# Performance work log

Measured on AMD Instinct MI355X. Metric: run time of the kernel, lower is better.

The kernel has to match this reference:

```python
import jax, jax.numpy as jnp
import numpy as np

SEQ = 2048
DIM = 4096
N_HEADS = 32
N_KV_HEADS = 8
HEAD_DIM = DIM // N_HEADS  # 128
ROPE_THETA = 500000.0


def setup_inputs() -> dict:
    key = jax.random.key(0)
    ks = jax.random.split(key, 5)
    s = 0.02  # keep activations numerically tame
    return {
        "x": jax.random.normal(ks[0], (SEQ, DIM), dtype=jnp.float32),
        "wq": jax.random.normal(ks[1], (DIM, DIM), dtype=jnp.float32) * s,
        "wk": jax.random.normal(ks[2], (N_KV_HEADS * HEAD_DIM, DIM), dtype=jnp.float32) * s,
        "wv": jax.random.normal(ks[3], (N_KV_HEADS * HEAD_DIM, DIM), dtype=jnp.float32) * s,
        "wo": jax.random.normal(ks[4], (DIM, DIM), dtype=jnp.float32) * s,
    }


def _rope(t):
    # t: [S, H, D]; pairs (t[...,2i], t[...,2i+1]) rotated by angle pos * theta^(-i/(D/2)),
    # matching torch.view_as_complex on x.view(S, -1, 2) * polar(1, pos*freq).
    S, H, D = t.shape
    half = D // 2
    freqs = 1.0 / (ROPE_THETA ** (jnp.arange(half, dtype=jnp.float32) / half))
    ang = jnp.arange(S, dtype=jnp.float32)[:, None] * freqs[None, :]  # [S, half]
    cos = jnp.cos(ang)[:, None, :]  # [S, 1, half]
    sin = jnp.sin(ang)[:, None, :]
    tr = t.reshape(S, H, half, 2)
    x0, x1 = tr[..., 0], tr[..., 1]
    r0 = x0 * cos - x1 * sin
    r1 = x0 * sin + x1 * cos
    return jnp.stack([r0, r1], axis=-1).reshape(S, H, D)


def reference(x, wq, wk, wv, wo):
    S = x.shape[0]
    group = N_HEADS // N_KV_HEADS
    # Per-head projections (batched over heads instead of python loop)
    q = jnp.einsum("sd,hkd->shk", x, wq.reshape(N_HEADS, HEAD_DIM, DIM))        # [S,H,D]
    k = jnp.einsum("sd,hkd->shk", x, wk.reshape(N_KV_HEADS, HEAD_DIM, DIM))     # [S,Hkv,D]
    v = jnp.einsum("sd,hkd->shk", x, wv.reshape(N_KV_HEADS, HEAD_DIM, DIM))     # [S,Hkv,D]
    q = _rope(q)
    k = _rope(k)
    # GQA: q head h uses kv head h // group -> repeat kv heads consecutively
    kf = jnp.repeat(k, group, axis=1)  # [S,H,D]
    vf = jnp.repeat(v, group, axis=1)  # [S,H,D]
    scores = jnp.einsum("shd,thd->hst", q, kf) / jnp.sqrt(jnp.float32(HEAD_DIM))
    causal = jnp.tril(jnp.ones((S, S), dtype=bool))
    scores = jnp.where(causal[None], scores, -jnp.inf)
    probs = jax.nn.softmax(scores, axis=-1)
    out = jnp.einsum("hst,thd->shd", probs, vf).reshape(S, N_HEADS * HEAD_DIM)
    return out @ wo.T
```

## Files before the change

### kernel.cpp

```cpp
#include <hip/hip_runtime.h>
#include <stdint.h>
#include <math.h>

#define SEQ   2048
#define DIM   4096
#define NHEAD 32
#define NKV   8
#define HD    128
#define KVDIM (NKV*HD)

typedef __bf16 bf16x8 __attribute__((ext_vector_type(8)));
typedef float  f32x4  __attribute__((ext_vector_type(4)));

__device__ __forceinline__ uint16_t f2bf(float f) {
  uint32_t u = __float_as_uint(f);
  uint32_t r = (u + 0x7FFFu + ((u >> 16) & 1u)) >> 16;
  return (uint16_t)r;
}
__device__ __forceinline__ bf16x8 ld_frag(const uint16_t* p) {
  return *(const bf16x8*)p;
}
__device__ __forceinline__ void async_cp16(const void* g, void* lds) {
  __builtin_amdgcn_global_load_lds(
      (const __attribute__((address_space(1))) void*)g,
      (__attribute__((address_space(3))) void*)lds, 16, 0, 0);
}
__device__ __forceinline__ uint32_t lds_u32(const void* p) {
  return (uint32_t)(uintptr_t)(const __attribute__((address_space(3))) void*)p;
}
__device__ __forceinline__ bf16x8 ds_read_b128a(uint32_t addr) {
  f32x4 r;
  asm volatile("ds_read_b128 %0, %1" : "=v"(r) : "v"(addr));
  return __builtin_bit_cast(bf16x8, r);
}

__global__ __launch_bounds__(256) void k_conv_all(
    const float* __restrict__ x, const float* __restrict__ wq,
    const float* __restrict__ wk, const float* __restrict__ wv,
    uint16_t* __restrict__ xb, uint16_t* __restrict__ wqkvb) {
  size_t i = (size_t)blockIdx.x * 256 + threadIdx.x;
  const float* s; uint16_t* d; size_t off;
  if (i < 2097152)      { s = x;  d = xb;                 off = i; }
  else if (i < 6291456) { s = wq; d = wqkvb;              off = i - 2097152; }
  else if (i < 7340032) { s = wk; d = wqkvb + 16777216u;  off = i - 6291456; }
  else                  { s = wv; d = wqkvb + 20971520u;  off = i - 7340032; }
  const float4 v = ((const float4*)s)[off];
  ushort4 o;
  o.x = f2bf(v.x); o.y = f2bf(v.y); o.z = f2bf(v.z); o.w = f2bf(v.w);
  ((ushort4*)d)[off] = o;
}

__global__ __launch_bounds__(256) void k_conv(const float* __restrict__ s,
                                              uint16_t* __restrict__ d, int n4) {
  int i = blockIdx.x * 256 + threadIdx.x;
  if (i >= n4) return;
  const float4 v = ((const float4*)s)[i];
  ushort4 o;
  o.x = f2bf(v.x); o.y = f2bf(v.y); o.z = f2bf(v.z); o.w = f2bf(v.w);
  ((ushort4*)d)[i] = o;
}


#define STG32(Tn) do {                                                          \
    const int _rg = ((Tn) & 3) * 8192;                                          \
    async_cp16(gA + (size_t)crow * DIM + (size_t)(Tn) * 32 + cs * 8,            \
               sA + _rg + tid * 8);                                             \
    async_cp16(gA + (size_t)(crow + 128) * DIM + (size_t)(Tn) * 32 + cs * 8,    \
               sA + _rg + 4096 + tid * 8);                                      \
    async_cp16(gB + (size_t)crow * DIM + (size_t)(Tn) * 32 + cs * 8,            \
               sB + _rg + tid * 8);                                             \
    async_cp16(gB + (size_t)(crow + 128) * DIM + (size_t)(Tn) * 32 + cs * 8,    \
               sB + _rg + 4096 + tid * 8);                                      \
  } while (0)

#define READ12(AF, BF, ringoff) do {                                            \
    _Pragma("unroll")                                                           \
    for (int _t = 0; _t < 8; _t++) AF[_t] = ds_read_b128a(offA[_t] + (ringoff));\
    _Pragma("unroll")                                                           \
    for (int _u = 0; _u < 4; _u++) BF[_u] = ds_read_b128a(offB[_u] + (ringoff));\
  } while (0)

#define MFMA32(AF, BF)                                                          \
    _Pragma("unroll")                                                           \
    for (int _t = 0; _t < 8; _t++)                                              \
      _Pragma("unroll")                                                         \
      for (int _u = 0; _u < 4; _u++)                                            \
        acc[_t][_u] = __builtin_amdgcn_mfma_f32_16x16x32_bf16(AF[_t], BF[_u],   \
                                                              acc[_t][_u], 0, 0, 0);

#define BODY(CA, CB, NA, NB, T) do {                                            \
    if ((T) + 3 < 128) STG32((T) + 3);                                          \
    if ((T) + 1 < 128) {                                                        \
      const uint32_t _ro = (uint32_t)((((T) + 1) & 3) << 14);                   \
      READ12(NA, NB, _ro);                                                      \
      asm volatile("s_waitcnt lgkmcnt(12)" ::: "memory");                       \
    } else {                                                                    \
      asm volatile("s_waitcnt lgkmcnt(0)" ::: "memory");                        \
    }                                                                           \
    __builtin_amdgcn_sched_barrier(0);                                          \
    __builtin_amdgcn_s_setprio(1);                                              \
    MFMA32(CA, CB);                                                             \
    __builtin_amdgcn_s_setprio(0);                                              \
    if ((T) + 3 < 128) { asm volatile("s_waitcnt vmcnt(4)" ::: "memory"); }     \
    else               { asm volatile("s_waitcnt vmcnt(0)" ::: "memory"); }     \
    if ((T) < 127) __builtin_amdgcn_s_barrier();                                \
  } while (0)

#define G256_PROLOGUE(Aptr, Bptr)                                               \
  __shared__ __align__(16) uint16_t sA[4 * 8192];                               \
  __shared__ __align__(16) uint16_t sB[4 * 8192];                               \
  const int tid  = threadIdx.x;                                                 \
  const int lane = tid & 63;                                                    \
  const int wv   = tid >> 6;                                                    \
  const int quad = lane >> 4;                                                   \
  const int l16  = lane & 15;                                                   \
  const int wm   = (wv >> 2) << 7;                                \
  const int wn   = (wv & 3) << 6;                             \
  const uint16_t* gA = Aptr + (size_t)m0 * DIM;                                 \
  const uint16_t* gB = Bptr + (size_t)n0 * DIM;                                 \
  const int crow = tid >> 2;                                                    \
  const int cs   = (tid & 3) ^ ((crow >> 1) & 3);                               \
  const uint32_t sAb = lds_u32(sA);                                             \
  const uint32_t sBb = lds_u32(sB);                                             \
  uint32_t offA[8], offB[4];                                                    \
  _Pragma("unroll")                                                             \
  for (int t = 0; t < 8; t++) {                                                 \
    int r_ = wm + t * 16 + l16;                                                 \
    offA[t] = sAb + (uint32_t)(r_ * 64 + (quad ^ ((r_ >> 1) & 3)) * 16);        \
  }                                                                             \
  _Pragma("unroll")                                                             \
  for (int u = 0; u < 4; u++) {                                                 \
    int r_ = wn + u * 16 + l16;                                                 \
    offB[u] = sBb + (uint32_t)(r_ * 64 + (quad ^ ((r_ >> 1) & 3)) * 16);        \
  }                                                                             \
  f32x4 acc[8][4] = {};                                                         \
  bf16x8 afC[8], bfC[4], afN[8], bfN[4];                                        \
  STG32(0); STG32(1); STG32(2);                                                 \
  asm volatile("s_waitcnt vmcnt(4)" ::: "memory");        \
  __builtin_amdgcn_s_barrier();                                                 \
  READ12(afC, bfC, 0u);                                                         \
  for (int T = 0; T < 128; T += 2) {                                            \
    BODY(afC, bfC, afN, bfN, T);                                                \
    BODY(afN, bfN, afC, bfC, T + 1);                                            \
  }

__global__ __launch_bounds__(512, 2) void k_gemm_qkv(
    const uint16_t* __restrict__ xb, const uint16_t* __restrict__ wqkvb,
    uint16_t* __restrict__ Qb, uint16_t* __restrict__ Kb, uint16_t* __restrict__ Vb)
{
  const int bx = blockIdx.x;
  const int m0 = blockIdx.y * 256;
  const int n0 = bx * 256;
  G256_PROLOGUE(xb, wqkvb)

  const int region = (bx < 16) ? 0 : (bx < 20 ? 1 : 2);
  uint16_t* outp; int ldC, cbase;
  if (region == 0)      { outp = Qb; ldC = DIM;   cbase = n0; }
  else if (region == 1) { outp = Kb; ldC = KVDIM; cbase = n0 - 4096; }
  else                  { outp = Vb; ldC = KVDIM; cbase = n0 - 5120; }

  #pragma unroll
  for (int t = 0; t < 8; t++)
    #pragma unroll
    for (int u = 0; u < 4; u++) {
      const int col = cbase + wn + u * 16 + l16;
      const int d = col & 127;
      const float freq = expf(-0.20503693f * (float)(d >> 1));
      const float sgn = (d & 1) ? 1.0f : -1.0f;
      #pragma unroll
      for (int r = 0; r < 4; r++) {
        const int row = m0 + wm + t * 16 + quad * 4 + r;
        float v = acc[t][u][r];
        if (region < 2) {
          float p = __shfl_xor(v, 1, 64);
          float ang = (float)row * freq;
          float sn, cc2;
          sincosf(ang, &sn, &cc2);
          v = v * cc2 + p * sn * sgn;
        }
        outp[(size_t)row * ldC + col] = f2bf(v);
      }
    }
}

__global__ __launch_bounds__(512, 2) void k_gemm_o(
    const uint16_t* __restrict__ ab, const uint16_t* __restrict__ wob,
    float* __restrict__ out)
{
  const int m0 = blockIdx.y * 256;
  const int n0 = blockIdx.x * 256;
  G256_PROLOGUE(ab, wob)
  #pragma unroll
  for (int t = 0; t < 8; t++)
    #pragma unroll
    for (int u = 0; u < 4; u++)
      #pragma unroll
      for (int r = 0; r < 4; r++) {
        int row = m0 + wm + t * 16 + quad * 4 + r;
        int col = n0 + wn + u * 16 + l16;
        out[(size_t)row * DIM + col] = acc[t][u][r];
      }
}

__global__ __launch_bounds__(256) void k_vtrans(const uint16_t* __restrict__ Vb,
                                                uint16_t* __restrict__ VT) {
  __shared__ uint16_t t[64][72];
  const int s0 = blockIdx.x * 64;
  const int c0 = blockIdx.y * 64;
  const int tid = threadIdx.x;
  #pragma unroll
  for (int i = 0; i < 2; i++) {
    int idx = i * 256 + tid;
    int r = idx >> 3, ch = idx & 7;
    uint4 dv = *(const uint4*)(Vb + (size_t)(s0 + r) * KVDIM + c0 + ch * 8);
    *(uint4*)(&t[r][ch * 8]) = dv;
  }
  __syncthreads();
  const int kvh = c0 >> 7;
  const int dbase = c0 & 127;
  #pragma unroll
  for (int i = 0; i < 2; i++) {
    int idx = i * 256 + tid;
    int d = idx >> 3, sc = idx & 7;
    uint16_t tmp[8];
    #pragma unroll
    for (int j2 = 0; j2 < 8; j2++) tmp[j2] = t[sc * 8 + j2][d];
    *(uint4*)(VT + (size_t)kvh * HD * SEQ + (size_t)(dbase + d) * SEQ + s0 + sc * 8) = *(const uint4*)tmp;
  }
}

#define BKV 64
#define NPAIR 40
__device__ __constant__ uint8_t c_pair[NPAIR] = {
  12,16,20,24,28,29,32,33,36,37,40,41,44,45,46,48,49,50,52,53,54,56,57,58,60,61,62,63,
  8,25,42,59,
  4,21,38,55,
  0,17,34,51
};
__device__ __constant__ uint8_t c_base[16] = {0,1,2,3,4,6,8,10,12,15,18,21,24,28,32,36};

__global__ __launch_bounds__(256) void k_flash_split(
    const uint16_t* __restrict__ Qb, const uint16_t* __restrict__ Kb,
    const uint16_t* __restrict__ VT, uint16_t* __restrict__ Opart,
    float* __restrict__ ml)
{
  const int pair = c_pair[blockIdx.x];
  const int qt   = pair >> 2;
  const int seg  = pair & 3;
  const int h    = blockIdx.y;
  const int kvh  = h >> 2;
  const int slot = h * NPAIR + c_base[qt] + seg;
  const int tid  = threadIdx.x;
  const int lane = tid & 63;
  const int wv   = tid >> 6;
  const int quad = lane >> 4;
  const int l16  = lane & 15;
  const int q0   = qt * 128;

  __shared__ __align__(16) uint16_t sK[BKV * 128];
  __shared__ __align__(16) uint16_t sVT[HD * BKV];
  __shared__ __align__(16) uint16_t sP[4 * 32 * 72];

  const uint16_t* Kbase  = Kb + kvh * HD;
  const uint16_t* VTbase = VT + (size_t)kvh * HD * SEQ;

  bf16x8 qf[2][4];
  #pragma unroll
  for (int mt = 0; mt < 2; mt++)
    #pragma unroll
    for (int ks = 0; ks < 4; ks++)
      qf[mt][ks] = ld_frag(Qb + (size_t)(q0 + wv * 32 + mt * 16 + l16) * DIM + h * HD + ks * 32 + quad * 8);

  __align__(16) uint16_t ones_bits[8];
  #pragma unroll
  for (int j = 0; j < 8; j++) ones_bits[j] = (l16 == 0) ? 0x3F80 : 0;
  const bf16x8 onesf = *(const bf16x8*)ones_bits;

  f32x4 Oacc[2][8] = {};
  f32x4 Lacc[2] = {};

  const float scale = 0.08838834764831845f;
  const float MFIX = 12.0f;
  const int j0 = seg * 8;
  const int j1 = min(j0 + 8, 2 * (qt + 1));

  for (int j = j0; j < j1; j++) {
    const int t0 = j * BKV;
    #pragma unroll
    for (int i = 0; i < 4; i++) {
      int pos = i * 256 + tid;
      int row = pos >> 4, g = (pos & 15) ^ (row & 7);
      async_cp16(Kbase + (size_t)(t0 + row) * KVDIM + g * 8, sK + pos * 8);
      int vrow = pos >> 3, vg = (pos & 7) ^ (vrow & 7);
      async_cp16(VTbase + (size_t)vrow * SEQ + t0 + vg * 8, sVT + pos * 8);
    }
    __syncthreads();

    bool active = (t0 <= q0 + wv * 32 + 31);
    if (active) {
      f32x4 Sacc[2][4] = {};
      #pragma unroll
      for (int ks = 0; ks < 4; ks++) {
        bf16x8 kf[4];
        #pragma unroll
        for (int nt = 0; nt < 4; nt++)
          kf[nt] = ld_frag(sK + (nt * 16 + l16) * 128 + (((ks * 4 + quad) ^ (l16 & 7)) * 8));
        #pragma unroll
        for (int mt = 0; mt < 2; mt++)
          #pragma unroll
          for (int nt = 0; nt < 4; nt++)
            Sacc[mt][nt] = __builtin_amdgcn_mfma_f32_16x16x32_bf16(qf[mt][ks], kf[nt], Sacc[mt][nt], 0, 0, 0);
      }
      const bool diag = (t0 + BKV - 1) > (q0 + wv * 32);
      #pragma unroll
      for (int mt = 0; mt < 2; mt++)
        #pragma unroll
        for (int nt = 0; nt < 4; nt++)
          #pragma unroll
          for (int r = 0; r < 4; r++) {
            float sv = Sacc[mt][nt][r] * scale - MFIX;
            bool msk = false;
            if (diag) {
              int qg = q0 + wv * 32 + mt * 16 + quad * 4 + r;
              int tg = t0 + nt * 16 + l16;
              msk = tg > qg;
            }
            float pv = msk ? 0.0f : __expf(sv);
            sP[(wv * 32 + mt * 16 + quad * 4 + r) * 72 + nt * 16 + l16] = f2bf(pv);
          }
      #pragma unroll
      for (int ks = 0; ks < 2; ks++) {
        bf16x8 pf[2], vf[8];
        #pragma unroll
        for (int mt = 0; mt < 2; mt++)
          pf[mt] = ld_frag(sP + (wv * 32 + mt * 16 + l16) * 72 + ks * 32 + quad * 8);
        #pragma unroll
        for (int dt = 0; dt < 8; dt++)
          vf[dt] = ld_frag(sVT + (dt * 16 + l16) * 64 + (((ks * 4 + quad) ^ (l16 & 7)) * 8));
        #pragma unroll
        for (int mt = 0; mt < 2; mt++) {
          Lacc[mt] = __builtin_amdgcn_mfma_f32_16x16x32_bf16(pf[mt], onesf, Lacc[mt], 0, 0, 0);
          #pragma unroll
          for (int dt = 0; dt < 8; dt++)
            Oacc[mt][dt] = __builtin_amdgcn_mfma_f32_16x16x32_bf16(pf[mt], vf[dt], Oacc[mt][dt], 0, 0, 0);
        }
      }
    }
    __syncthreads();
  }

  uint16_t* Op = Opart + (size_t)slot * (128 * 128);
  #pragma unroll
  for (int mt = 0; mt < 2; mt++)
    #pragma unroll
    for (int r = 0; r < 4; r++) {
      int row = wv * 32 + mt * 16 + quad * 4 + r;
      #pragma unroll
      for (int dt = 0; dt < 8; dt++)
        Op[row * 128 + dt * 16 + l16] = f2bf(Oacc[mt][dt][r]);
      if (l16 == 0)
        ml[(size_t)slot * 128 + row] = Lacc[mt][r];
    }
}

__global__ __launch_bounds__(256) void k_combine(
    const uint16_t* __restrict__ Opart, const float* __restrict__ ml,
    uint16_t* __restrict__ attnb)
{
  const int qt = blockIdx.x;
  const int h  = blockIdx.y;
  const int nseg = (qt >> 2) + 1;
  const int slot0 = h * NPAIR + c_base[qt];
  const int tid = threadIdx.x;
  const int row = tid >> 1;
  const int dh  = (tid & 1) * 64;

  float L = 0.0f;
  #pragma unroll
  for (int i = 0; i < 4; i++)
    if (i < nseg) L += ml[(size_t)(slot0 + i) * 128 + row];
  const float invL = 1.0f / L;

  uint16_t* dst = attnb + (size_t)(qt * 128 + row) * DIM + h * HD + dh;
  #pragma unroll
  for (int c = 0; c < 8; c++) {
    int d = dh + c * 8;
    float acc[8] = {};
    #pragma unroll
    for (int i = 0; i < 4; i++) {
      if (i < nseg) {
        bf16x8 v = ld_frag(Opart + (size_t)(slot0 + i) * (128 * 128) + row * 128 + d);
        #pragma unroll
        for (int j = 0; j < 8; j++) acc[j] += (float)v[j];
      }
    }
    uint16_t outv[8];
    #pragma unroll
    for (int j = 0; j < 8; j++) outv[j] = f2bf(acc[j] * invL);
    *(uint4*)(dst + c * 8) = *(const uint4*)outv;
  }
}

extern "C" void kernel_launch(void* const* d_in, const int* in_sizes, int n_in,
                              void* d_out, int out_size, void* d_ws, size_t ws_size,
                              hipStream_t stream) {
  const float* x  = (const float*)d_in[0];
  const float* wq = (const float*)d_in[1];
  const float* wk = (const float*)d_in[2];
  const float* wv = (const float*)d_in[3];
  const float* wo = (const float*)d_in[4];
  float* out = (float*)d_out;

  uint8_t* ws = (uint8_t*)d_ws;
  uint16_t* xb     = (uint16_t*)(ws + 0);
  uint16_t* wqkvb  = (uint16_t*)(ws + 16777216ull);
  uint16_t* Qb     = (uint16_t*)(ws + 67108864ull);
  uint16_t* Kb     = (uint16_t*)(ws + 83886080ull);
  uint16_t* Vb     = (uint16_t*)(ws + 88080384ull);
  uint16_t* VT     = (uint16_t*)(ws + 16777216ull);
  uint16_t* Opart  = (uint16_t*)(ws + 20971520ull);
  float*    mlbuf  = (float*)   (ws + 62914560ull);
  uint16_t* wob    = (uint16_t*)(ws + 16777216ull);
  uint16_t* attnb  = xb;

  k_conv_all<<<32768, 256, 0, stream>>>(x, wq, wk, wv, xb, wqkvb);
  k_gemm_qkv<<<dim3(24, 8), 512, 0, stream>>>(xb, wqkvb, Qb, Kb, Vb);
  k_vtrans<<<dim3(32, 16), 256, 0, stream>>>(Vb, VT);
  k_flash_split<<<dim3(NPAIR, 32), 256, 0, stream>>>(Qb, Kb, VT, Opart, mlbuf);
  k_combine<<<dim3(16, 32), 256, 0, stream>>>(Opart, mlbuf, attnb);
  k_conv<<<16384, 256, 0, stream>>>(wo, wob, 4194304);
  k_gemm_o<<<dim3(16, 8), 512, 0, stream>>>(attnb, wob, out);
}
```

Before: 611.5 us.

## Rewrite output-projection GEMM with 128x256 tiles and 4-stage async LDS pipeline

The O-projection GEMM moves from 256x256 tiles on 128 blocks to 128x256 tiles on 256 blocks, so more of the GPU's compute units get work. It adds a custom 4-buffer async global-to-LDS pipeline that keeps three stages in flight. Fragment reads are double-buffered in registers and timed with explicit waitcnt and sched barriers, and MFMA issue priority is raised. Smaller tiles re-read more of the A and B operands, and the hand-scheduled wait counts add a correctness risk if they are wrong.

```diff
diff --git a/kernel.cpp b/kernel.cpp
--- a/kernel.cpp
+++ b/kernel.cpp
@@ -183,15 +183,93 @@
     }
 }
 
+
+#define O_STG(Tn) do {                                                          \
+    const int _ra = ((Tn) & 3) * 4096;                                          \
+    const int _rb = ((Tn) & 3) * 8192;                                          \
+    async_cp16(gA + (size_t)crow * DIM + (size_t)(Tn) * 32 + cs * 8,            \
+               sA + _ra + tid * 8);                                             \
+    async_cp16(gB + (size_t)crow * DIM + (size_t)(Tn) * 32 + cs * 8,            \
+               sB + _rb + tid * 8);                                             \
+    async_cp16(gB + (size_t)(crow + 128) * DIM + (size_t)(Tn) * 32 + cs * 8,    \
+               sB + _rb + 4096 + tid * 8);                                      \
+  } while (0)
+
+#define O_BODY(CA, CB, NA, NB, T) do {                                          \
+    if ((T) + 3 < 128) O_STG((T) + 3);                                          \
+    if ((T) + 1 < 128) {                                                        \
+      const uint32_t _ra = (uint32_t)((((T) + 1) & 3) << 13);                   \
+      const uint32_t _rb = (uint32_t)((((T) + 1) & 3) << 14);                   \
+      _Pragma("unroll")                                                         \
+      for (int _t = 0; _t < 4; _t++) NA[_t] = ds_read_b128a(offA[_t] + _ra);    \
+      _Pragma("unroll")                                                         \
+      for (int _u = 0; _u < 4; _u++) NB[_u] = ds_read_b128a(offB[_u] + _rb);    \
+      asm volatile("s_waitcnt lgkmcnt(8)" ::: "memory");                        \
+    } else {                                                                    \
+      asm volatile("s_waitcnt lgkmcnt(0)" ::: "memory");                        \
+    }                                                                           \
+    __builtin_amdgcn_sched_barrier(0);                                          \
+    __builtin_amdgcn_s_setprio(1);                                              \
+    _Pragma("unroll")                                                           \
+    for (int _t = 0; _t < 4; _t++)                                              \
+      _Pragma("unroll")                                                         \
+      for (int _u = 0; _u < 4; _u++)                                            \
+        acc[_t][_u] = __builtin_amdgcn_mfma_f32_16x16x32_bf16(CA[_t], CB[_u],   \
+                                                              acc[_t][_u], 0, 0, 0); \
+    __builtin_amdgcn_s_setprio(0);                                              \
+    if ((T) + 3 < 128) { asm volatile("s_waitcnt vmcnt(3)" ::: "memory"); }     \
+    else               { asm volatile("s_waitcnt vmcnt(0)" ::: "memory"); }     \
+    if ((T) < 127) __builtin_amdgcn_s_barrier();                                \
+  } while (0)
+
 __global__ __launch_bounds__(512, 2) void k_gemm_o(
     const uint16_t* __restrict__ ab, const uint16_t* __restrict__ wob,
     float* __restrict__ out)
 {
-  const int m0 = blockIdx.y * 256;
+  __shared__ __align__(16) uint16_t sA[4 * 4096];
+  __shared__ __align__(16) uint16_t sB[4 * 8192];
+  const int m0 = blockIdx.y * 128;
   const int n0 = blockIdx.x * 256;
-  G256_PROLOGUE(ab, wob)
-  #pragma unroll
-  for (int t = 0; t < 8; t++)
+  const int tid  = threadIdx.x;
+  const int lane = tid & 63;
+  const int wv   = tid >> 6;
+  const int quad = lane >> 4;
+  const int l16  = lane & 15;
+  const int wm   = (wv >> 2) << 6;
+  const int wn   = (wv & 3) << 6;
+  const uint16_t* gA = ab  + (size_t)m0 * DIM;
+  const uint16_t* gB = wob + (size_t)n0 * DIM;
+  const int crow = tid >> 2;
+  const int cs   = (tid & 3) ^ ((crow >> 1) & 3);
+  const uint32_t sAb = lds_u32(sA);
+  const uint32_t sBb = lds_u32(sB);
+  uint32_t offA[4], offB[4];
+  #pragma unroll
+  for (int t = 0; t < 4; t++) {
+    int r_ = wm + t * 16 + l16;
+    offA[t] = sAb + (uint32_t)(r_ * 64 + (quad ^ ((r_ >> 1) & 3)) * 16);
+  }
+  #pragma unroll
+  for (int u = 0; u < 4; u++) {
+    int r_ = wn + u * 16 + l16;
+    offB[u] = sBb + (uint32_t)(r_ * 64 + (quad ^ ((r_ >> 1) & 3)) * 16);
+  }
+  f32x4 acc[4][4] = {};
+  bf16x8 afC[4], bfC[4], afN[4], bfN[4];
+  O_STG(0); O_STG(1); O_STG(2);
+  asm volatile("s_waitcnt vmcnt(3)" ::: "memory");
+  __builtin_amdgcn_s_barrier();
+  #pragma unroll
+  for (int _t = 0; _t < 4; _t++) afC[_t] = ds_read_b128a(offA[_t]);
+  #pragma unroll
+  for (int _u = 0; _u < 4; _u++) bfC[_u] = ds_read_b128a(offB[_u]);
+  for (int T = 0; T < 128; T += 2) {
+    O_BODY(afC, bfC, afN, bfN, T);
+    O_BODY(afN, bfN, afC, bfC, T + 1);
+  }
+  asm volatile("s_waitcnt vmcnt(0)" ::: "memory");
+  #pragma unroll
+  for (int t = 0; t < 4; t++)
     #pragma unroll
     for (int u = 0; u < 4; u++)
       #pragma unroll
@@ -429,5 +507,5 @@
   k_flash_split<<<dim3(NPAIR, 32), 256, 0, stream>>>(Qb, Kb, VT, Opart, mlbuf);
   k_combine<<<dim3(16, 32), 256, 0, stream>>>(Opart, mlbuf, attnb);
   k_conv<<<16384, 256, 0, stream>>>(wo, wob, 4194304);
-  k_gemm_o<<<dim3(16, 8), 512, 0, stream>>>(attnb, wob, out);
-}
+  k_gemm_o<<<dim3(16, 16), 512, 0, stream>>>(attnb, wob, out);
+}
```

Measured after the change: 574.8 us. -6.0%, faster.
